# Kernel optimization log

Measured on AMD Instinct MI355X. Metric: run time of the kernel, lower is better.

The kernel has to match this reference:

```python
import jax, jax.numpy as jnp
import numpy as np

B, R, E, K = 32, 8192, 256, 64

def setup_inputs() -> dict:
    key = jax.random.key(0)
    kx, kc = jax.random.split(key)
    x = jax.random.normal(kx, (B, R, E), dtype=jnp.float32)
    # orthonormal cluster centers (equivalent to Gram-Schmidt init in the module)
    c0 = jax.random.normal(kc, (E, K), dtype=jnp.float32)
    q, _ = jnp.linalg.qr(c0)          # (E, K) with orthonormal columns
    centers = q.T                      # (K, E), rows orthonormal
    return {"x": x, "centers": centers}

def reference(x, centers):
    # x: (B, R, E); centers: (K, E)
    scores = jnp.einsum('bre,ke->brk', x, centers)   # (B, R, K)
    p = jax.nn.softmax(scores, axis=-1)              # soft assignments over clusters
    z = jnp.einsum('brk,bre->bke', p, x)             # (B, K, E)
    return z
```

## Files before the change

### kernel.cpp

```cpp
#include <hip/hip_runtime.h>
#include <hip/hip_bf16.h>

#define BB 32
#define RR 8192
#define EE 256
#define KK 64

#define BPB 16
#define ROWS_PB (RR / BPB)
#define TILE 32
#define NT (ROWS_PB / TILE)
#define RPAD 40

typedef __attribute__((ext_vector_type(8))) short short8;
typedef __attribute__((ext_vector_type(4))) float f32x4;

__device__ __forceinline__ unsigned short bf16rn(float v) {
    unsigned int u = __builtin_bit_cast(unsigned int, v);
    u = (u + 0x7FFFu + ((u >> 16) & 1u)) >> 16;
    return (unsigned short)u;
}
__device__ __forceinline__ float bf2f(unsigned short h) {
    unsigned int u = ((unsigned int)h) << 16;
    return __builtin_bit_cast(float, u);
}

__global__ __launch_bounds__(256, 2) void cluster_mfma(
    const float* __restrict__ x, const float* __restrict__ c,
    float* __restrict__ z, float* __restrict__ ws, int use_ws)
{
    __shared__ unsigned short xh[TILE * 256];
    __shared__ unsigned short xl[TILE * 256];
    __shared__ unsigned short pth[KK * RPAD];
    __shared__ unsigned short ptl[KK * RPAD];
    __shared__ float redm[4][TILE];
    __shared__ float reds[4][TILE];

    char* const xhb = (char*)xh;
    char* const xlb = (char*)xl;

    const int t = threadIdx.x;
    const int w = t >> 6;
    const int l = t & 63;
    const int n = l & 15;
    const int g = l >> 4;
    const int b = blockIdx.y;
    const int blk = blockIdx.x;

    const float* xb = x + (size_t)b * RR * EE;

    short8 chf[8], clf[8];
    {
        const float* crow = c + (size_t)(16 * w + n) * EE + 8 * g;
        #pragma unroll
        for (int e0 = 0; e0 < 8; ++e0) {
            const float* p = crow + e0 * 32;
            float4 v0 = *(const float4*)(p);
            float4 v1 = *(const float4*)(p + 4);
            float vv[8] = {v0.x, v0.y, v0.z, v0.w, v1.x, v1.y, v1.z, v1.w};
            #pragma unroll
            for (int j = 0; j < 8; ++j) {
                unsigned short h = bf16rn(vv[j]);
                chf[e0][j] = (short)h;
                clf[e0][j] = (short)bf16rn(vv[j] - bf2f(h));
            }
        }
    }

    f32x4 zacc[4][4];
    #pragma unroll
    for (int i = 0; i < 4; ++i)
        #pragma unroll
        for (int j = 0; j < 4; ++j)
            zacc[i][j] = (f32x4){0.f, 0.f, 0.f, 0.f};

    const int rs = t >> 3;
    const int qs = t & 7;
    const int swzs = (rs & 7) << 4;
    const int swzn = (n & 7) << 4;

    for (int tile = 0; tile < NT; ++tile) {
        const int r0 = blk * ROWS_PB + tile * TILE;

        {
            const float* srow = xb + (size_t)(r0 + rs) * EE;
            #pragma unroll
            for (int j4 = 0; j4 < 8; ++j4) {
                float4 v = *(const float4*)(srow + qs * 4 + j4 * 32);
                float vv[4] = {v.x, v.y, v.z, v.w};
                unsigned long long uh = 0, ul = 0;
                #pragma unroll
                for (int j = 0; j < 4; ++j) {
                    unsigned short h  = bf16rn(vv[j]);
                    unsigned short lo = bf16rn(vv[j] - bf2f(h));
                    uh |= ((unsigned long long)h)  << (16 * j);
                    ul |= ((unsigned long long)lo) << (16 * j);
                }
                const int off = (rs * 512 + qs * 8 + j4 * 64) ^ swzs;
                *(unsigned long long*)(xhb + off) = uh;
                *(unsigned long long*)(xlb + off) = ul;
            }
        }
        __syncthreads();

        f32x4 sacc[2];
        sacc[0] = (f32x4){0.f, 0.f, 0.f, 0.f};
        sacc[1] = (f32x4){0.f, 0.f, 0.f, 0.f};
        #pragma unroll
        for (int e0 = 0; e0 < 8; ++e0) {
            #pragma unroll
            for (int cc = 0; cc < 2; ++cc) {
                const int row = cc * 16 + n;
                const int off = (row * 512 + e0 * 64 + g * 16) ^ swzn;
                short8 xvh = *(const short8*)(xhb + off);
                short8 xvl = *(const short8*)(xlb + off);
                sacc[cc] = __builtin_amdgcn_mfma_f32_16x16x32_bf16(chf[e0], xvh, sacc[cc], 0, 0, 0);
                sacc[cc] = __builtin_amdgcn_mfma_f32_16x16x32_bf16(chf[e0], xvl, sacc[cc], 0, 0, 0);
                sacc[cc] = __builtin_amdgcn_mfma_f32_16x16x32_bf16(clf[e0], xvh, sacc[cc], 0, 0, 0);
            }
        }

        float mx[2], sm[2];
        #pragma unroll
        for (int cc = 0; cc < 2; ++cc) {
            float m = fmaxf(fmaxf(sacc[cc][0], sacc[cc][1]), fmaxf(sacc[cc][2], sacc[cc][3]));
            m = fmaxf(m, __shfl_xor(m, 16));
            m = fmaxf(m, __shfl_xor(m, 32));
            mx[cc] = m;
        }
        if (l < 16) { redm[w][n] = mx[0]; redm[w][16 + n] = mx[1]; }
        __syncthreads();
        float M[2];
        M[0] = fmaxf(fmaxf(redm[0][n], redm[1][n]), fmaxf(redm[2][n], redm[3][n]));
        M[1] = fmaxf(fmaxf(redm[0][16 + n], redm[1][16 + n]),
                     fmaxf(redm[2][16 + n], redm[3][16 + n]));
        float ex[2][4];
        #pragma unroll
        for (int cc = 0; cc < 2; ++cc) {
            float s = 0.f;
            #pragma unroll
            for (int r = 0; r < 4; ++r) { ex[cc][r] = __expf(sacc[cc][r] - M[cc]); s += ex[cc][r]; }
            s += __shfl_xor(s, 16);
            s += __shfl_xor(s, 32);
            sm[cc] = s;
        }
        if (l < 16) { reds[w][n] = sm[0]; reds[w][16 + n] = sm[1]; }
        __syncthreads();
        float R[2];
        R[0] = 1.0f / (reds[0][n] + reds[1][n] + reds[2][n] + reds[3][n]);
        R[1] = 1.0f / (reds[0][16 + n] + reds[1][16 + n] + reds[2][16 + n] + reds[3][16 + n]);

        #pragma unroll
        for (int cc = 0; cc < 2; ++cc) {
            #pragma unroll
            for (int r = 0; r < 4; ++r) {
                float p = ex[cc][r] * R[cc];
                unsigned short ph = bf16rn(p);
                unsigned short pl = bf16rn(p - bf2f(ph));
                const int k  = 16 * w + 4 * g + r;
                const int rl = 16 * cc + n;
                pth[k * RPAD + rl] = ph;
                ptl[k * RPAD + rl] = pl;
            }
        }
        __syncthreads();

        short8 pah[4], pal[4];
        #pragma unroll
        for (int kc = 0; kc < 4; ++kc) {
            const int off = ((16 * kc + n) * RPAD + 8 * g) * 2;
            pah[kc] = *(const short8*)((char*)pth + off);
            pal[kc] = *(const short8*)((char*)ptl + off);
        }
        #pragma unroll
        for (int ecl = 0; ecl < 4; ++ecl) {
            const int ebyte = (64 * w + 16 * ecl + n) * 2;
            short8 xvh, xvl;
            #pragma unroll
            for (int j = 0; j < 8; ++j) {
                const int row = 8 * g + j;
                const int off = (row * 512 + ebyte) ^ ((row & 7) << 4);
                xvh[j] = (short)*(const unsigned short*)(xhb + off);
                xvl[j] = (short)*(const unsigned short*)(xlb + off);
            }
            #pragma unroll
            for (int kc = 0; kc < 4; ++kc) {
                zacc[kc][ecl] = __builtin_amdgcn_mfma_f32_16x16x32_bf16(pah[kc], xvh, zacc[kc][ecl], 0, 0, 0);
                zacc[kc][ecl] = __builtin_amdgcn_mfma_f32_16x16x32_bf16(pah[kc], xvl, zacc[kc][ecl], 0, 0, 0);
                zacc[kc][ecl] = __builtin_amdgcn_mfma_f32_16x16x32_bf16(pal[kc], xvh, zacc[kc][ecl], 0, 0, 0);
            }
        }
        __syncthreads();
    }

    if (use_ws) {
        float* dst = ws + (size_t)(b * BPB + blk) * KK * EE;
        #pragma unroll
        for (int kc = 0; kc < 4; ++kc)
            #pragma unroll
            for (int r = 0; r < 4; ++r)
                #pragma unroll
                for (int ecl = 0; ecl < 4; ++ecl)
                    dst[(size_t)(16 * kc + 4 * g + r) * EE + 64 * w + 16 * ecl + n] =
                        zacc[kc][ecl][r];
    } else {
        float* zb = z + (size_t)b * KK * EE;
        for (int kc = 0; kc < 4; ++kc)
            for (int r = 0; r < 4; ++r)
                for (int ecl = 0; ecl < 4; ++ecl)
                    atomicAdd(&zb[(size_t)(16 * kc + 4 * g + r) * EE + 64 * w + 16 * ecl + n],
                              zacc[kc][ecl][r]);
    }
}

__global__ __launch_bounds__(256) void reduce_partials(
    const float* __restrict__ ws, float* __restrict__ z)
{
    const int idx = blockIdx.x * 256 + threadIdx.x;
    const int b   = idx / (KK * EE);
    const int rem = idx - b * (KK * EE);
    const float* p = ws + (size_t)b * BPB * KK * EE + rem;
    float s = 0.0f;
    #pragma unroll
    for (int i = 0; i < BPB; ++i) s += p[(size_t)i * KK * EE];
    z[idx] = s;
}

extern "C" void kernel_launch(void* const* d_in, const int* in_sizes, int n_in,
                              void* d_out, int out_size, void* d_ws, size_t ws_size,
                              hipStream_t stream) {
    (void)in_sizes; (void)n_in;
    const float* x = (const float*)d_in[0];
    const float* c = (const float*)d_in[1];
    float* z  = (float*)d_out;
    float* ws = (float*)d_ws;

    const size_t need = (size_t)BB * BPB * KK * EE * sizeof(float);
    const int use_ws = (ws_size >= need) ? 1 : 0;

    if (!use_ws)
        hipMemsetAsync(d_out, 0, (size_t)out_size * sizeof(float), stream);

    dim3 grid(BPB, BB);
    hipLaunchKernelGGL(cluster_mfma, grid, dim3(256), 0, stream, x, c, z, ws, use_ws);

    if (use_ws) {
        const int nel = BB * KK * EE;
        hipLaunchKernelGGL(reduce_partials, dim3(nel / 256), dim3(256), 0, stream, ws, z);
    }
}
```

Before: 385.8 us.

## Prefetch next x tile, merge softmax reductions, improve swizzle, vectorize reduce

Loads the next tile of x into registers before the MFMA work on the current tile, so global load latency overlaps compute. Merges the per-wave max and sum reductions into one shared-memory exchange with online rescaling, which removes one __syncthreads per tile. Changes the LDS XOR swizzle to also mix higher row bits, aimed at bank conflicts in the transposed column reads. Vectorizes the partial-sum reduction kernel to float4. The prefetch costs 32 extra VGPRs per thread, which could hurt occupancy under launch_bounds(256,2).

```diff
diff --git a/kernel.cpp b/kernel.cpp
--- a/kernel.cpp
+++ b/kernel.cpp
@@ -23,6 +23,9 @@
 __device__ __forceinline__ float bf2f(unsigned short h) {
     unsigned int u = ((unsigned int)h) << 16;
     return __builtin_bit_cast(float, u);
+}
+__device__ __forceinline__ int swzb(int row) {
+    return ((row ^ (row >> 3)) & 7) << 4;
 }
 
 __global__ __launch_bounds__(256, 2) void cluster_mfma(
@@ -76,18 +79,22 @@
 
     const int rs = t >> 3;
     const int qs = t & 7;
-    const int swzs = (rs & 7) << 4;
-    const int swzn = (n & 7) << 4;
-
+    const int swzs = swzb(rs);
+
+    float4 pf[8];
+    {
+        const float* srow = xb + (size_t)(blk * ROWS_PB + rs) * EE;
+        #pragma unroll
+        for (int j4 = 0; j4 < 8; ++j4)
+            pf[j4] = *(const float4*)(srow + qs * 4 + j4 * 32);
+    }
+
+    #pragma unroll 1
     for (int tile = 0; tile < NT; ++tile) {
-        const int r0 = blk * ROWS_PB + tile * TILE;
-
         {
-            const float* srow = xb + (size_t)(r0 + rs) * EE;
             #pragma unroll
             for (int j4 = 0; j4 < 8; ++j4) {
-                float4 v = *(const float4*)(srow + qs * 4 + j4 * 32);
-                float vv[4] = {v.x, v.y, v.z, v.w};
+                float vv[4] = {pf[j4].x, pf[j4].y, pf[j4].z, pf[j4].w};
                 unsigned long long uh = 0, ul = 0;
                 #pragma unroll
                 for (int j = 0; j < 4; ++j) {
@@ -101,6 +108,12 @@
                 *(unsigned long long*)(xlb + off) = ul;
             }
         }
+        if (tile + 1 < NT) {
+            const float* srow = xb + (size_t)(blk * ROWS_PB + (tile + 1) * TILE + rs) * EE;
+            #pragma unroll
+            for (int j4 = 0; j4 < 8; ++j4)
+                pf[j4] = *(const float4*)(srow + qs * 4 + j4 * 32);
+        }
         __syncthreads();
 
         f32x4 sacc[2];
@@ -111,7 +124,7 @@
             #pragma unroll
             for (int cc = 0; cc < 2; ++cc) {
                 const int row = cc * 16 + n;
-                const int off = (row * 512 + e0 * 64 + g * 16) ^ swzn;
+                const int off = (row * 512 + e0 * 64 + g * 16) ^ swzb(row);
                 short8 xvh = *(const short8*)(xhb + off);
                 short8 xvl = *(const short8*)(xlb + off);
                 sacc[cc] = __builtin_amdgcn_mfma_f32_16x16x32_bf16(chf[e0], xvh, sacc[cc], 0, 0, 0);
@@ -120,41 +133,42 @@
             }
         }
 
-        float mx[2], sm[2];
+        float Mw[2], Sw[2], ex[2][4];
         #pragma unroll
         for (int cc = 0; cc < 2; ++cc) {
             float m = fmaxf(fmaxf(sacc[cc][0], sacc[cc][1]), fmaxf(sacc[cc][2], sacc[cc][3]));
             m = fmaxf(m, __shfl_xor(m, 16));
             m = fmaxf(m, __shfl_xor(m, 32));
-            mx[cc] = m;
-        }
-        if (l < 16) { redm[w][n] = mx[0]; redm[w][16 + n] = mx[1]; }
-        __syncthreads();
-        float M[2];
-        M[0] = fmaxf(fmaxf(redm[0][n], redm[1][n]), fmaxf(redm[2][n], redm[3][n]));
-        M[1] = fmaxf(fmaxf(redm[0][16 + n], redm[1][16 + n]),
-                     fmaxf(redm[2][16 + n], redm[3][16 + n]));
-        float ex[2][4];
-        #pragma unroll
-        for (int cc = 0; cc < 2; ++cc) {
+            Mw[cc] = m;
             float s = 0.f;
             #pragma unroll
-            for (int r = 0; r < 4; ++r) { ex[cc][r] = __expf(sacc[cc][r] - M[cc]); s += ex[cc][r]; }
+            for (int r = 0; r < 4; ++r) { ex[cc][r] = __expf(sacc[cc][r] - m); s += ex[cc][r]; }
             s += __shfl_xor(s, 16);
             s += __shfl_xor(s, 32);
-            sm[cc] = s;
-        }
-        if (l < 16) { reds[w][n] = sm[0]; reds[w][16 + n] = sm[1]; }
-        __syncthreads();
-        float R[2];
-        R[0] = 1.0f / (reds[0][n] + reds[1][n] + reds[2][n] + reds[3][n]);
-        R[1] = 1.0f / (reds[0][16 + n] + reds[1][16 + n] + reds[2][16 + n] + reds[3][16 + n]);
-
+            Sw[cc] = s;
+        }
+        if (l < 16) {
+            redm[w][n] = Mw[0]; redm[w][16 + n] = Mw[1];
+            reds[w][n] = Sw[0]; reds[w][16 + n] = Sw[1];
+        }
+        __syncthreads();
+        float scale[2];
         #pragma unroll
         for (int cc = 0; cc < 2; ++cc) {
+            const int row = 16 * cc + n;
+            const float m0 = redm[0][row], m1 = redm[1][row];
+            const float m2 = redm[2][row], m3 = redm[3][row];
+            const float M = fmaxf(fmaxf(m0, m1), fmaxf(m2, m3));
+            const float S = reds[0][row] * __expf(m0 - M) + reds[1][row] * __expf(m1 - M)
+                          + reds[2][row] * __expf(m2 - M) + reds[3][row] * __expf(m3 - M);
+            scale[cc] = __expf(Mw[cc] - M) / S;
+        }
+
+        #pragma unroll
+        for (int cc = 0; cc < 2; ++cc) {
             #pragma unroll
             for (int r = 0; r < 4; ++r) {
-                float p = ex[cc][r] * R[cc];
+                float p = ex[cc][r] * scale[cc];
                 unsigned short ph = bf16rn(p);
                 unsigned short pl = bf16rn(p - bf2f(ph));
                 const int k  = 16 * w + 4 * g + r;
@@ -179,7 +193,7 @@
             #pragma unroll
             for (int j = 0; j < 8; ++j) {
                 const int row = 8 * g + j;
-                const int off = (row * 512 + ebyte) ^ ((row & 7) << 4);
+                const int off = (row * 512 + ebyte) ^ swzb(row);
                 xvh[j] = (short)*(const unsigned short*)(xhb + off);
                 xvl[j] = (short)*(const unsigned short*)(xlb + off);
             }
@@ -216,14 +230,18 @@
 __global__ __launch_bounds__(256) void reduce_partials(
     const float* __restrict__ ws, float* __restrict__ z)
 {
-    const int idx = blockIdx.x * 256 + threadIdx.x;
-    const int b   = idx / (KK * EE);
-    const int rem = idx - b * (KK * EE);
-    const float* p = ws + (size_t)b * BPB * KK * EE + rem;
-    float s = 0.0f;
+    const int idx4 = blockIdx.x * 256 + threadIdx.x;
+    const int per_b = KK * EE / 4;
+    const int b   = idx4 / per_b;
+    const int rem = idx4 - b * per_b;
+    const float4* p = (const float4*)ws + (size_t)b * BPB * per_b + rem;
+    float4 s = {0.f, 0.f, 0.f, 0.f};
     #pragma unroll
-    for (int i = 0; i < BPB; ++i) s += p[(size_t)i * KK * EE];
-    z[idx] = s;
+    for (int i = 0; i < BPB; ++i) {
+        float4 v = p[(size_t)i * per_b];
+        s.x += v.x; s.y += v.y; s.z += v.z; s.w += v.w;
+    }
+    ((float4*)z)[idx4] = s;
 }
 
 extern "C" void kernel_launch(void* const* d_in, const int* in_sizes, int n_in,
@@ -245,7 +263,7 @@
     hipLaunchKernelGGL(cluster_mfma, grid, dim3(256), 0, stream, x, c, z, ws, use_ws);
 
     if (use_ws) {
-        const int nel = BB * KK * EE;
-        hipLaunchKernelGGL(reduce_partials, dim3(nel / 256), dim3(256), 0, stream, ws, z);
-    }
-}
+        const int nel4 = BB * KK * EE / 4;
+        hipLaunchKernelGGL(reduce_partials, dim3(nel4 / 256), dim3(256), 0, stream, ws, z);
+    }
+}
```

After: 452.7 us. +17.3%, slower.
